# Performance work log

Hardware: AMD Instinct MI355X
Metric: run time of the kernel (lower is better)

Reference implementation:

```python
import jax, jax.numpy as jnp
import numpy as np

B, P = 65536, 22  # sets, max players per freeze frame
IN, HID, OUT = 6, 64, 128


def setup_inputs() -> dict:
    key = jax.random.key(0)
    k0, k1, k2, k3, k4, k5 = jax.random.split(key, 6)
    pitch = jnp.array([120.0, 80.0], dtype=jnp.float32)
    player_locs = jax.random.uniform(k0, (B, P, 2), dtype=jnp.float32) * pitch
    actor_locs = jax.random.uniform(k1, (B, 2), dtype=jnp.float32) * pitch
    # teammate / keeper flags in {0,1}
    flags = jax.random.randint(k2, (B, P, 2), 0, 2).astype(jnp.float32)
    # validity mask: 0 -> player skipped (simulates ragged / missing entries)
    mask = jax.random.randint(k3, (B, P), 0, 2).astype(jnp.int32)
    W1 = jax.random.normal(k4, (IN, HID), dtype=jnp.float32) / np.sqrt(IN)
    b1 = jnp.zeros((HID,), dtype=jnp.float32)
    W2 = jax.random.normal(k5, (HID, OUT), dtype=jnp.float32) / np.sqrt(HID)
    b2 = jnp.zeros((OUT,), dtype=jnp.float32)
    return {"player_locs": player_locs, "actor_locs": actor_locs, "flags": flags,
            "mask": mask, "W1": W1, "b1": b1, "W2": W2, "b2": b2}


def reference(player_locs, actor_locs, flags, mask, W1, b1, W2, b2):
    # per-player features relative to the actor: [dx, dy, dist, angle, teammate, keeper]
    dxy = player_locs - actor_locs[:, None, :]                 # [B,P,2]
    dist = jnp.sqrt(jnp.sum(dxy * dxy, axis=-1, keepdims=True))  # [B,P,1]
    angle = jnp.arctan2(dxy[..., 1:2], dxy[..., 0:1])            # [B,P,1]
    feats = jnp.concatenate([dxy, dist, angle, flags], axis=-1)  # [B,P,6]
    # PlayerMLP: Linear -> ReLU -> Linear
    h = jax.nn.relu(jnp.einsum('bpi,ih->bph', feats, W1) + b1)   # [B,P,64]
    emb = jnp.einsum('bph,ho->bpo', h, W2) + b2                  # [B,P,128]
    # masked mean over valid players; empty sets yield zeros (sum is 0)
    m = mask.astype(emb.dtype)[..., None]                        # [B,P,1]
    cnt = jnp.sum(m, axis=1)                                     # [B,1]
    pooled = jnp.sum(emb * m, axis=1) / jnp.maximum(cnt, 1.0)    # [B,128]
    return pooled
```

## Files before the change

kernel.cpp:

```cpp
#include <hip/hip_runtime.h>
#include <math.h>

#define PMAX 22
#define HID 64
#define OUTD 128
#define SETS_PER_WAVE 16
#define WAVES_PER_BLOCK 4

typedef __attribute__((ext_vector_type(4))) float float4v;
typedef _Float16 fh2 __attribute__((ext_vector_type(2)));
typedef _Float16 half8 __attribute__((ext_vector_type(8)));

__device__ __forceinline__ int rl_i(int v, int l) {
    return __builtin_amdgcn_readlane(v, l);
}
__device__ __forceinline__ int pk2(float x, float y) {
    auto v = __builtin_amdgcn_cvt_pkrtz(x, y);
    union { decltype(v) h; int i; } c;
    c.h = v;
    return c.i;
}
__device__ __forceinline__ unsigned short f16b(float x) {
    return (unsigned short)(pk2(x, x) & 0xFFFF);
}
__device__ __forceinline__ float fdot2i(int a, int b, float c) {
    union { int i; fh2 h; } ua, ub;
    ua.i = a;
    ub.i = b;
#if defined(__has_builtin) && __has_builtin(__builtin_amdgcn_fdot2)
    return __builtin_amdgcn_fdot2(ua.h, ub.h, c, false);
#else
    return fmaf((float)ua.h.x, (float)ub.h.x, fmaf((float)ua.h.y, (float)ub.h.y, c));
#endif
}
__device__ __forceinline__ void wave_lds_sync() {
    asm volatile("s_waitcnt lgkmcnt(0)" ::: "memory");
    __builtin_amdgcn_wave_barrier();
}
__device__ __forceinline__ float fast_atan2(float y, float x) {
    float ax = fabsf(x), ay = fabsf(y);
    float mn = fminf(ax, ay), mx = fmaxf(ax, ay);
    float a = mn * __builtin_amdgcn_rcpf(fmaxf(mx, 1e-30f));
    float s = a * a;
    float r = a * fmaf(s, fmaf(s, fmaf(s, -0.0851330f, 0.1801410f), -0.3302995f), 0.9998660f);
    if (ay > ax) r = 1.57079637f - r;
    if (x < 0.0f) r = 3.14159274f - r;
    return copysignf(r, y);
}

__global__ __launch_bounds__(256, 4) void set_encoder_kernel(
    const float* __restrict__ player_locs,
    const float* __restrict__ actor_locs,
    const float* __restrict__ flags,
    const int*   __restrict__ mask,
    const float* __restrict__ W1,
    const float* __restrict__ b1,
    const float* __restrict__ W2,
    const float* __restrict__ b2,
    float* __restrict__ out)
{
    __shared__ __align__(16) unsigned w2f[16 * 256];
    __shared__ __align__(16) unsigned short hb[WAVES_PER_BLOCK][SETS_PER_WAVE][72];

    const int tid  = threadIdx.x;
    const int lane = tid & 63;
    const int wave = tid >> 6;

    const int wave_id = blockIdx.x * WAVES_PER_BLOCK + wave;
    const int set0    = wave_id * SETS_PER_WAVE;

    {
        const int pr = tid >> 3;
        const int nt = tid & 7;
        const float* rA = W2 + (size_t)(2 * pr) * OUTD + 16 * nt;
        const float* rB = rA + OUTD;
        float ra[16], rb[16];
#pragma unroll
        for (int i = 0; i < 4; ++i) {
            *(float4*)&ra[4 * i] = ((const float4*)rA)[i];
            *(float4*)&rb[4 * i] = ((const float4*)rB)[i];
        }
        const int kt = pr >> 4;
        const int kk = (2 * pr) & 31;
        const int Q  = kk >> 3;
        const int j2 = (kk >> 1) & 3;
        const int base = ((kt * 8 + nt) * 4 + Q) * 64 + j2;
#pragma unroll
        for (int c = 0; c < 16; ++c)
            w2f[base + 4 * c] = pk2(ra[c], rb[c]);
    }

    const int w01 = pk2(W1[0 * HID + lane], W1[1 * HID + lane]);
    const int w23 = pk2(W1[2 * HID + lane], W1[3 * HID + lane]);
    const int w45 = pk2(W1[4 * HID + lane], W1[5 * HID + lane]);
    const float b1l = b1[lane];

    __syncthreads();

    int fh[8][3];
    unsigned long long bm[8];
    {
        const int lidx = lane < 2 * PMAX ? lane : 2 * PMAX - 1;
        const size_t r0 = (size_t)set0 * PMAX + lidx;
        const float2* plb = (const float2*)player_locs + r0;
        const float2* flb = (const float2*)flags + r0;
        const int*    mkb = mask + r0;
        const float2* acb = (const float2*)actor_locs + set0 + (lidx >= PMAX ? 1 : 0);
#pragma unroll
        for (int g = 0; g < 8; ++g) {
            float2 pl = plb[g * 2 * PMAX];
            float2 fl = flb[g * 2 * PMAX];
            int    m  = mkb[g * 2 * PMAX];
            float2 ac = acb[2 * g];
            float dx = pl.x - ac.x;
            float dy = pl.y - ac.y;
            float dist = __builtin_amdgcn_sqrtf(fmaf(dx, dx, dy * dy));
            float ang  = fast_atan2(dy, dx);
            fh[g][0] = pk2(dx, dy);
            fh[g][1] = pk2(dist, ang);
            fh[g][2] = pk2(fl.x, fl.y);
            bm[g] = __ballot((lane < 2 * PMAX) && (m != 0));
        }
    }

    unsigned nonempty = 0;
#pragma unroll
    for (int s = 0; s < SETS_PER_WAVE; ++s) {
        const int g    = s >> 1;
        const int base = (s & 1) * PMAX;
        unsigned bits = (unsigned)(bm[g] >> base) & 0x3FFFFFu;
        const int cnt = __builtin_popcount(bits);
        if (bits) nonempty |= (1u << s);
        float acc = 0.0f;
        unsigned bb = bits;
        while (bb) {
            const int p = __builtin_ctz(bb);
            bb &= bb - 1;
            const int src = base + p;
            const int u0 = rl_i(fh[g][0], src);
            const int u1 = rl_i(fh[g][1], src);
            const int u2 = rl_i(fh[g][2], src);
            float t = fdot2i(u0, w01, b1l);
            t = fdot2i(u1, w23, t);
            t = fdot2i(u2, w45, t);
            acc += fmaxf(t, 0.0f);
        }
        const float hbar = acc * (1.0f / fmaxf((float)cnt, 1.0f));
        hb[wave][s][lane] = f16b(hbar);
    }
    wave_lds_sync();

    const int Q   = lane >> 4;
    const int c15 = lane & 15;
    half8 afrag[2];
#pragma unroll
    for (int kt = 0; kt < 2; ++kt) {
        union { uint4 u4; half8 h8; } cv;
        cv.u4 = *(const uint4*)&hb[wave][c15][kt * 32 + Q * 8];
        afrag[kt] = cv.h8;
    }

    float4v acc[8];
#pragma unroll
    for (int nt = 0; nt < 8; ++nt) {
        union { uint4 u4; half8 h8; } f0, f1;
        f0.u4 = *(const uint4*)&w2f[(0 * 8 + nt) * 256 + 4 * lane];
        f1.u4 = *(const uint4*)&w2f[(1 * 8 + nt) * 256 + 4 * lane];
        float4v z = {0.0f, 0.0f, 0.0f, 0.0f};
        acc[nt] = __builtin_amdgcn_mfma_f32_16x16x32_f16(afrag[0], f0.h8, z, 0, 0, 0);
        acc[nt] = __builtin_amdgcn_mfma_f32_16x16x32_f16(afrag[1], f1.h8, acc[nt], 0, 0, 0);
    }

    float fs[4];
#pragma unroll
    for (int r = 0; r < 4; ++r) fs[r] = (float)((nonempty >> (4 * Q + r)) & 1u);

    const float* b2b = b2 + c15;
    float b2v[8];
#pragma unroll
    for (int nt = 0; nt < 8; ++nt) b2v[nt] = b2b[16 * nt];

    float* obase = out + (size_t)(set0 + 4 * Q) * OUTD + c15;
#pragma unroll
    for (int nt = 0; nt < 8; ++nt) {
#pragma unroll
        for (int r = 0; r < 4; ++r)
            obase[r * OUTD + nt * 16] = fmaf(fs[r], b2v[nt], acc[nt][r]);
    }
}

extern "C" void kernel_launch(void* const* d_in, const int* in_sizes, int n_in,
                              void* d_out, int out_size, void* d_ws, size_t ws_size,
                              hipStream_t stream) {
    const float* player_locs = (const float*)d_in[0];
    const float* actor_locs  = (const float*)d_in[1];
    const float* flags       = (const float*)d_in[2];
    const int*   mask        = (const int*)d_in[3];
    const float* W1          = (const float*)d_in[4];
    const float* b1          = (const float*)d_in[5];
    const float* W2          = (const float*)d_in[6];
    const float* b2          = (const float*)d_in[7];
    float*       out         = (float*)d_out;

    const int B = in_sizes[0] / (PMAX * 2);
    const int sets_per_block = WAVES_PER_BLOCK * SETS_PER_WAVE;
    const int grid = (B + sets_per_block - 1) / sets_per_block;

    hipLaunchKernelGGL(set_encoder_kernel, dim3(grid), dim3(256), 0, stream,
                       player_locs, actor_locs, flags, mask, W1, b1, W2, b2, out);
}
```

Measured before the change: 113.1 us.

## Halve sets per wave and unroll player loop by two for ILP

Each wave now processes 8 sets instead of 16, doubling the number of waves and blocks. The MFMA A operand rows are duplicated (lane&7), and only half the lanes write output. The per-set player loop is unrolled in pairs so two independent dot-product chains overlap readlane latency. The launch-bounds occupancy hint is removed. The cost is wasted MFMA work on duplicated rows and the W2 LDS staging repeated across twice as many blocks.

```diff
diff --git a/kernel.cpp b/kernel.cpp
--- a/kernel.cpp
+++ b/kernel.cpp
@@ -4,7 +4,7 @@
 #define PMAX 22
 #define HID 64
 #define OUTD 128
-#define SETS_PER_WAVE 16
+#define SETS_PER_WAVE 8
 #define WAVES_PER_BLOCK 4
 
 typedef __attribute__((ext_vector_type(4))) float float4v;
@@ -48,7 +48,7 @@
     return copysignf(r, y);
 }
 
-__global__ __launch_bounds__(256, 4) void set_encoder_kernel(
+__global__ __launch_bounds__(256) void set_encoder_kernel(
     const float* __restrict__ player_locs,
     const float* __restrict__ actor_locs,
     const float* __restrict__ flags,
@@ -97,8 +97,8 @@
 
     __syncthreads();
 
-    int fh[8][3];
-    unsigned long long bm[8];
+    int fh[4][3];
+    unsigned long long bm[4];
     {
         const int lidx = lane < 2 * PMAX ? lane : 2 * PMAX - 1;
         const size_t r0 = (size_t)set0 * PMAX + lidx;
@@ -107,7 +107,7 @@
         const int*    mkb = mask + r0;
         const float2* acb = (const float2*)actor_locs + set0 + (lidx >= PMAX ? 1 : 0);
 #pragma unroll
-        for (int g = 0; g < 8; ++g) {
+        for (int g = 0; g < 4; ++g) {
             float2 pl = plb[g * 2 * PMAX];
             float2 fl = flb[g * 2 * PMAX];
             int    m  = mkb[g * 2 * PMAX];
@@ -133,16 +133,29 @@
         if (bits) nonempty |= (1u << s);
         float acc = 0.0f;
         unsigned bb = bits;
-        while (bb) {
+        const int npair = cnt >> 1;
+        for (int i = 0; i < npair; ++i) {
+            const int p0 = __builtin_ctz(bb); bb &= bb - 1;
+            const int p1 = __builtin_ctz(bb); bb &= bb - 1;
+            const int s0 = base + p0, s1 = base + p1;
+            const int a0 = rl_i(fh[g][0], s0), b0 = rl_i(fh[g][0], s1);
+            const int a1 = rl_i(fh[g][1], s0), b1v = rl_i(fh[g][1], s1);
+            const int a2 = rl_i(fh[g][2], s0), b2v = rl_i(fh[g][2], s1);
+            float t0 = fdot2i(a0, w01, b1l);
+            float t1 = fdot2i(b0, w01, b1l);
+            t0 = fdot2i(a1, w23, t0);
+            t1 = fdot2i(b1v, w23, t1);
+            t0 = fdot2i(a2, w45, t0);
+            t1 = fdot2i(b2v, w45, t1);
+            acc += fmaxf(t0, 0.0f);
+            acc += fmaxf(t1, 0.0f);
+        }
+        if (cnt & 1) {
             const int p = __builtin_ctz(bb);
-            bb &= bb - 1;
             const int src = base + p;
-            const int u0 = rl_i(fh[g][0], src);
-            const int u1 = rl_i(fh[g][1], src);
-            const int u2 = rl_i(fh[g][2], src);
-            float t = fdot2i(u0, w01, b1l);
-            t = fdot2i(u1, w23, t);
-            t = fdot2i(u2, w45, t);
+            float t = fdot2i(rl_i(fh[g][0], src), w01, b1l);
+            t = fdot2i(rl_i(fh[g][1], src), w23, t);
+            t = fdot2i(rl_i(fh[g][2], src), w45, t);
             acc += fmaxf(t, 0.0f);
         }
         const float hbar = acc * (1.0f / fmaxf((float)cnt, 1.0f));
@@ -152,11 +165,12 @@
 
     const int Q   = lane >> 4;
     const int c15 = lane & 15;
+    const int sA  = lane & 7;
     half8 afrag[2];
 #pragma unroll
     for (int kt = 0; kt < 2; ++kt) {
         union { uint4 u4; half8 h8; } cv;
-        cv.u4 = *(const uint4*)&hb[wave][c15][kt * 32 + Q * 8];
+        cv.u4 = *(const uint4*)&hb[wave][sA][kt * 32 + Q * 8];
         afrag[kt] = cv.h8;
     }
 
@@ -171,21 +185,23 @@
         acc[nt] = __builtin_amdgcn_mfma_f32_16x16x32_f16(afrag[1], f1.h8, acc[nt], 0, 0, 0);
     }
 
-    float fs[4];
-#pragma unroll
-    for (int r = 0; r < 4; ++r) fs[r] = (float)((nonempty >> (4 * Q + r)) & 1u);
-
-    const float* b2b = b2 + c15;
-    float b2v[8];
-#pragma unroll
-    for (int nt = 0; nt < 8; ++nt) b2v[nt] = b2b[16 * nt];
-
-    float* obase = out + (size_t)(set0 + 4 * Q) * OUTD + c15;
-#pragma unroll
-    for (int nt = 0; nt < 8; ++nt) {
-#pragma unroll
-        for (int r = 0; r < 4; ++r)
-            obase[r * OUTD + nt * 16] = fmaf(fs[r], b2v[nt], acc[nt][r]);
+    if (Q < 2) {
+        float fs[4];
+#pragma unroll
+        for (int r = 0; r < 4; ++r) fs[r] = (float)((nonempty >> (4 * Q + r)) & 1u);
+
+        const float* b2b = b2 + c15;
+        float b2v[8];
+#pragma unroll
+        for (int nt = 0; nt < 8; ++nt) b2v[nt] = b2b[16 * nt];
+
+        float* obase = out + (size_t)(set0 + 4 * Q) * OUTD + c15;
+#pragma unroll
+        for (int nt = 0; nt < 8; ++nt) {
+#pragma unroll
+            for (int r = 0; r < 4; ++r)
+                obase[r * OUTD + nt * 16] = fmaf(fs[r], b2v[nt], acc[nt][r]);
+        }
     }
 }
 
```

After: 110.8 us. 1.02x faster.
